# Kernel tuning notes

Hardware: AMD Instinct MI355X
Metric: run time of the kernel (lower is better)

The kernel has to match this reference:

```python
import jax, jax.numpy as jnp
import numpy as np

N_NODES = 50000
N_EDGES = 800000
IN_DIM_N = 128
IN_DIM_E = 32
OUT_DIM = 128


def setup_inputs() -> dict:
    key = jax.random.key(0)
    k = jax.random.split(key, 6)
    nfeats = jax.random.normal(k[0], (N_NODES, IN_DIM_N), dtype=jnp.float32)
    efeats = jax.random.normal(k[1], (N_EDGES, IN_DIM_E), dtype=jnp.float32)
    # xavier-normal-ish scaling
    W_fc = jax.random.normal(k[2], (OUT_DIM, IN_DIM_N), dtype=jnp.float32) * (2.0 / np.sqrt(IN_DIM_N + OUT_DIM))
    W_attn = jax.random.normal(k[3], (1, 2 * OUT_DIM + IN_DIM_E), dtype=jnp.float32) * 0.08
    src = jax.random.randint(k[4], (N_EDGES,), 0, N_NODES, dtype=jnp.int32)
    dst = jax.random.randint(k[5], (N_EDGES,), 0, N_NODES, dtype=jnp.int32)
    return {"nfeats": nfeats, "efeats": efeats, "W_fc": W_fc, "W_attn": W_attn, "src": src, "dst": dst}


def reference(nfeats, efeats, W_fc, W_attn, src, dst):
    n_nodes = nfeats.shape[0]
    out_dim = W_fc.shape[0]
    in_dim_e = efeats.shape[1]

    # z = fc(nfeats)  [N, out_dim]
    z = nfeats @ W_fc.T

    # attn_fc(cat([z_src, efeats, z_dst])) split into three small dots
    a = W_attn[0]
    a_src = a[:out_dim]
    a_e = a[out_dim:out_dim + in_dim_e]
    a_dst = a[out_dim + in_dim_e:]
    s_src = z @ a_src            # [N]
    s_dst = z @ a_dst            # [N]
    s_e = efeats @ a_e           # [E]

    # per-edge attention logit + leaky_relu (torch default slope 0.01)
    e = jax.nn.leaky_relu(s_src[src] + s_e + s_dst[dst], negative_slope=0.01)  # [E]

    # segment softmax over incoming edges of each dst node
    m = jax.ops.segment_max(e, dst, num_segments=n_nodes)
    m = jnp.where(jnp.isfinite(m), m, 0.0)  # guard zero-degree nodes
    w = jnp.exp(e - m[dst])
    denom = jax.ops.segment_sum(w, dst, num_segments=n_nodes)
    alpha = w / jnp.where(denom > 0, denom, 1.0)[dst]  # [E]

    # weighted sum of source z into dst nodes
    h = jax.ops.segment_sum(alpha[:, None] * z[src], dst, num_segments=n_nodes)  # [N, out_dim]
    return h
```

## Files before the change

kernel.cpp:

```cpp
#include <hip/hip_runtime.h>
#include <math.h>

#define N_NODES 50000
#define N_EDGES 800000
#define IN_DIM_N 128
#define IN_DIM_E 32
#define OUT_DIM 128
#define SCAN_BLOCKS ((N_NODES + 255) / 256)
#define GEMM_BLOCKS ((N_NODES + 63) / 64)

typedef __bf16 bf16x8 __attribute__((ext_vector_type(8)));
typedef float  f32x4  __attribute__((ext_vector_type(4)));

__device__ inline unsigned bf16_rne(float x) {
    unsigned u = __float_as_uint(x);
    return (u + 0x7FFFu + ((u >> 16) & 1u)) >> 16;
}
__device__ inline unsigned pack_bf2(float a, float b) {
    return bf16_rne(a) | (bf16_rne(b) << 16);
}

__global__ void wfrag_kernel(const float* __restrict__ W, unsigned* __restrict__ Wfrag,
                             int* __restrict__ counts) {
    int t = blockIdx.x * 256 + threadIdx.x;
    for (int i = t; i < N_NODES; i += 2048) counts[i] = 0;
    if (t >= 2048) return;
    int lane = t & 63;
    int tile = (t >> 6) & 7;
    int ks   = t >> 9;
    int n  = tile * 16 + (lane & 15);
    int kb = ks * 32 + (lane >> 4) * 8;
    const float* srcp = W + n * 128 + kb;
    unsigned o[4];
#pragma unroll
    for (int j = 0; j < 4; ++j) o[j] = pack_bf2(srcp[2 * j], srcp[2 * j + 1]);
    ((uint4*)Wfrag)[t] = *(uint4*)o;
}

__global__ void hist_kernel(const int* __restrict__ dst, int* __restrict__ counts) {
    int i = blockIdx.x * blockDim.x + threadIdx.x;
    if (i < N_EDGES) atomicAdd(&counts[dst[i]], 1);
}

__launch_bounds__(256)
__global__ void gemm_mfma_kernel(const float* __restrict__ A, const unsigned* __restrict__ Wfrag,
                                 const float* __restrict__ attn, unsigned* __restrict__ zb,
                                 float* __restrict__ s_src, float* __restrict__ s_dst) {
    __shared__ unsigned Au[64 * 68];
    __shared__ float asrc[128], adst[128];
    int tid = threadIdx.x;
    int row0 = blockIdx.x * 64;

    if (tid < 128) { asrc[tid] = attn[tid]; adst[tid] = attn[160 + tid]; }

    for (int i = tid; i < 64 * 32; i += 256) {
        int r = i >> 5, q = i & 31;
        int gr = row0 + r;
        float4 v = make_float4(0.f, 0.f, 0.f, 0.f);
        if (gr < N_NODES) v = ((const float4*)A)[(long)gr * 32 + q];
        uint2 p = make_uint2(pack_bf2(v.x, v.y), pack_bf2(v.z, v.w));
        *((uint2*)&Au[r * 68 + q * 2]) = p;
    }
    __syncthreads();

    int lane = tid & 63;
    int wave = tid >> 6;
    int m = lane & 15, quad = lane >> 4;
    const uint4* Wg = (const uint4*)Wfrag;

    f32x4 acc[8];
#pragma unroll
    for (int t = 0; t < 8; ++t) acc[t] = (f32x4){0.f, 0.f, 0.f, 0.f};

#pragma unroll
    for (int ks = 0; ks < 4; ++ks) {
        uint4 au = *((const uint4*)&Au[(wave * 16 + m) * 68 + ks * 16 + quad * 4]);
        bf16x8 af = *(bf16x8*)&au;
#pragma unroll
        for (int t = 0; t < 8; ++t) {
            uint4 bu = Wg[(ks * 8 + t) * 64 + lane];
            bf16x8 bf = *(bf16x8*)&bu;
            acc[t] = __builtin_amdgcn_mfma_f32_16x16x32_bf16(af, bf, acc[t], 0, 0, 0);
        }
    }

    float ps[4] = {0.f, 0.f, 0.f, 0.f}, pd[4] = {0.f, 0.f, 0.f, 0.f};
#pragma unroll
    for (int t = 0; t < 8; ++t) {
        float as_ = asrc[t * 16 + m], ad_ = adst[t * 16 + m];
#pragma unroll
        for (int r = 0; r < 4; ++r) {
            float v = acc[t][r];
            ps[r] = fmaf(v, as_, ps[r]);
            pd[r] = fmaf(v, ad_, pd[r]);
            float vn = __shfl_xor(v, 1, 64);
            if (!(m & 1)) {
                int grow = row0 + wave * 16 + quad * 4 + r;
                if (grow < N_NODES)
                    zb[(long)grow * 64 + t * 8 + (m >> 1)] = pack_bf2(v, vn);
            }
        }
    }
#pragma unroll
    for (int r = 0; r < 4; ++r) {
        for (int off = 1; off < 16; off <<= 1) {
            ps[r] += __shfl_xor(ps[r], off, 64);
            pd[r] += __shfl_xor(pd[r], off, 64);
        }
    }
    if (m == 0) {
#pragma unroll
        for (int r = 0; r < 4; ++r) {
            int grow = row0 + wave * 16 + quad * 4 + r;
            if (grow < N_NODES) { s_src[grow] = ps[r]; s_dst[grow] = pd[r]; }
        }
    }
}

__launch_bounds__(256)
__global__ void scan1_kernel(const int* __restrict__ counts, int* __restrict__ offsets,
                             int* __restrict__ cursor, int* __restrict__ blocksums) {
    int i = blockIdx.x * 256 + threadIdx.x;
    int v = (i < N_NODES) ? counts[i] : 0;
    int lane = threadIdx.x & 63;
    int wv = threadIdx.x >> 6;
    int x = v;
    for (int off = 1; off < 64; off <<= 1) {
        int y = __shfl_up(x, off, 64);
        if (lane >= off) x += y;
    }
    __shared__ int wsum[4];
    if (lane == 63) wsum[wv] = x;
    __syncthreads();
    int base = 0;
    for (int w = 0; w < wv; ++w) base += wsum[w];
    int excl = base + x - v;
    if (i <= N_NODES) offsets[i] = excl;
    if (i < N_NODES) cursor[i] = excl;
    if (threadIdx.x == 255) blocksums[blockIdx.x] = base + x;
}

__launch_bounds__(256)
__global__ void scan2_kernel(int* __restrict__ blocksums) {
    int t = threadIdx.x;
    int v = (t < SCAN_BLOCKS) ? blocksums[t] : 0;
    int lane = t & 63;
    int wv = t >> 6;
    int x = v;
    for (int off = 1; off < 64; off <<= 1) {
        int y = __shfl_up(x, off, 64);
        if (lane >= off) x += y;
    }
    __shared__ int wsum[4];
    if (lane == 63) wsum[wv] = x;
    __syncthreads();
    int base = 0;
    for (int w = 0; w < wv; ++w) base += wsum[w];
    if (t < SCAN_BLOCKS) blocksums[t] = base + x - v;
}

__global__ void score_scatter_kernel(const float* __restrict__ efeats, const float* __restrict__ attn,
                                     const int* __restrict__ src, const int* __restrict__ dst,
                                     const float* __restrict__ s_src, const float* __restrict__ s_dst,
                                     int* __restrict__ cursor, const int* __restrict__ blocksums,
                                     unsigned* __restrict__ pairs4) {
    int i = blockIdx.x * blockDim.x + threadIdx.x;
    if (i >= N_EDGES) return;
    const float4* ef = (const float4*)(efeats + (long)i * IN_DIM_E);
    const float4* ae = (const float4*)(attn + OUT_DIM);
    float se = 0.f;
#pragma unroll
    for (int q = 0; q < IN_DIM_E / 4; ++q) {
        float4 v = ef[q];
        float4 a = ae[q];
        se += v.x * a.x + v.y * a.y + v.z * a.z + v.w * a.w;
    }
    int s = src[i], d = dst[i];
    float x = s_src[s] + se + s_dst[d];
    float ev = (x >= 0.f) ? x : 0.01f * x;
    float w = expf(ev);
    int pos = atomicAdd(&cursor[d], 1) + blocksums[d >> 8];
    pairs4[pos] = (unsigned)s | (bf16_rne(w) << 16);
}

__launch_bounds__(256)
__global__ void aggregate_kernel(const unsigned* __restrict__ pairs4, const int* __restrict__ offsets,
                                 const int* __restrict__ blocksums,
                                 const unsigned* __restrict__ zb, float* __restrict__ h) {
    int node = blockIdx.x * 4 + (threadIdx.x >> 6);
    if (node >= N_NODES) return;
    int lane = threadIdx.x & 63;
    int beg = offsets[node] + blocksums[node >> 8];
    int end = offsets[node + 1] + blocksums[(node + 1) >> 8];
    float ax0 = 0.f, ay0 = 0.f, ax1 = 0.f, ay1 = 0.f;
    float ax2 = 0.f, ay2 = 0.f, ax3 = 0.f, ay3 = 0.f;
    float dsum = 0.f;
    for (int base = beg; base < end; base += 64) {
        int n = min(64, end - base);
        unsigned u = 0;
        if (lane < n) {
            u = pairs4[base + lane];
            dsum += __uint_as_float(u & 0xFFFF0000u);
        }
        int j = 0;
        for (; j + 3 < n; j += 4) {
            unsigned u0 = (unsigned)__shfl((int)u, j, 64);
            unsigned u1 = (unsigned)__shfl((int)u, j + 1, 64);
            unsigned u2 = (unsigned)__shfl((int)u, j + 2, 64);
            unsigned u3 = (unsigned)__shfl((int)u, j + 3, 64);
            unsigned z0 = zb[(long)(u0 & 0xFFFFu) * 64 + lane];
            unsigned z1 = zb[(long)(u1 & 0xFFFFu) * 64 + lane];
            unsigned z2 = zb[(long)(u2 & 0xFFFFu) * 64 + lane];
            unsigned z3 = zb[(long)(u3 & 0xFFFFu) * 64 + lane];
            float w0 = __uint_as_float(u0 & 0xFFFF0000u);
            float w1 = __uint_as_float(u1 & 0xFFFF0000u);
            float w2 = __uint_as_float(u2 & 0xFFFF0000u);
            float w3 = __uint_as_float(u3 & 0xFFFF0000u);
            ax0 = fmaf(w0, __uint_as_float(z0 << 16), ax0);
            ay0 = fmaf(w0, __uint_as_float(z0 & 0xFFFF0000u), ay0);
            ax1 = fmaf(w1, __uint_as_float(z1 << 16), ax1);
            ay1 = fmaf(w1, __uint_as_float(z1 & 0xFFFF0000u), ay1);
            ax2 = fmaf(w2, __uint_as_float(z2 << 16), ax2);
            ay2 = fmaf(w2, __uint_as_float(z2 & 0xFFFF0000u), ay2);
            ax3 = fmaf(w3, __uint_as_float(z3 << 16), ax3);
            ay3 = fmaf(w3, __uint_as_float(z3 & 0xFFFF0000u), ay3);
        }
        for (; j < n; ++j) {
            unsigned u0 = (unsigned)__shfl((int)u, j, 64);
            unsigned z0 = zb[(long)(u0 & 0xFFFFu) * 64 + lane];
            float w0 = __uint_as_float(u0 & 0xFFFF0000u);
            ax0 = fmaf(w0, __uint_as_float(z0 << 16), ax0);
            ay0 = fmaf(w0, __uint_as_float(z0 & 0xFFFF0000u), ay0);
        }
    }
    float accx = (ax0 + ax1) + (ax2 + ax3);
    float accy = (ay0 + ay1) + (ay2 + ay3);
    for (int off = 32; off; off >>= 1) dsum += __shfl_xor(dsum, off, 64);
    float scale = 1.f / (dsum > 0.f ? dsum : 1.f);
    ((float2*)h)[(long)node * 64 + lane] = make_float2(accx * scale, accy * scale);
}

extern "C" void kernel_launch(void* const* d_in, const int* in_sizes, int n_in,
                              void* d_out, int out_size, void* d_ws, size_t ws_size,
                              hipStream_t stream) {
    const float* nfeats = (const float*)d_in[0];
    const float* efeats = (const float*)d_in[1];
    const float* W_fc   = (const float*)d_in[2];
    const float* W_attn = (const float*)d_in[3];
    const int*   src    = (const int*)d_in[4];
    const int*   dst    = (const int*)d_in[5];
    float* h = (float*)d_out;

    char* ws = (char*)d_ws;
    unsigned* zb     = (unsigned*)ws;
    float* s_src     = (float*)(ws + (size_t)N_NODES * 64 * 4);
    float* s_dst     = s_src + N_NODES;
    unsigned* Wfrag  = (unsigned*)(s_dst + N_NODES);
    int*   counts    = (int*)(Wfrag + 8192);
    int*   offsets   = counts + N_NODES;
    int*   cursor    = offsets + N_NODES + 4;
    int*   blocksums = cursor + N_NODES;
    unsigned* pairs4 = (unsigned*)(blocksums + SCAN_BLOCKS + 4);

    wfrag_kernel<<<8, 256, 0, stream>>>(W_fc, Wfrag, counts);
    hist_kernel<<<(N_EDGES + 255) / 256, 256, 0, stream>>>(dst, counts);
    gemm_mfma_kernel<<<GEMM_BLOCKS, 256, 0, stream>>>(
        nfeats, Wfrag, W_attn, zb, s_src, s_dst);
    scan1_kernel<<<SCAN_BLOCKS, 256, 0, stream>>>(counts, offsets, cursor, blocksums);
    scan2_kernel<<<1, 256, 0, stream>>>(blocksums);
    score_scatter_kernel<<<(N_EDGES + 255) / 256, 256, 0, stream>>>(
        efeats, W_attn, src, dst, s_src, s_dst, cursor, blocksums, pairs4);
    aggregate_kernel<<<(N_NODES + 3) / 4, 256, 0, stream>>>(pairs4, offsets, blocksums, zb, h);
}
```

Before: 309.1 us.

## Fuse edge scoring with histogram and record ranks for atomic-free scatter

```diff
diff --git a/kernel.cpp b/kernel.cpp
--- a/kernel.cpp
+++ b/kernel.cpp
@@ -37,11 +37,6 @@
     ((uint4*)Wfrag)[t] = *(uint4*)o;
 }
 
-__global__ void hist_kernel(const int* __restrict__ dst, int* __restrict__ counts) {
-    int i = blockIdx.x * blockDim.x + threadIdx.x;
-    if (i < N_EDGES) atomicAdd(&counts[dst[i]], 1);
-}
-
 __launch_bounds__(256)
 __global__ void gemm_mfma_kernel(const float* __restrict__ A, const unsigned* __restrict__ Wfrag,
                                  const float* __restrict__ attn, unsigned* __restrict__ zb,
@@ -117,9 +112,33 @@
     }
 }
 
+__global__ void edge_score_hist_kernel(const float* __restrict__ efeats, const float* __restrict__ attn,
+                                       const int* __restrict__ src, const int* __restrict__ dst,
+                                       const float* __restrict__ s_src, const float* __restrict__ s_dst,
+                                       int* __restrict__ counts, unsigned short* __restrict__ ranks,
+                                       unsigned short* __restrict__ wq) {
+    int i = blockIdx.x * blockDim.x + threadIdx.x;
+    if (i >= N_EDGES) return;
+    const float4* ef = (const float4*)(efeats + (long)i * IN_DIM_E);
+    const float4* ae = (const float4*)(attn + OUT_DIM);
+    float se = 0.f;
+#pragma unroll
+    for (int q = 0; q < IN_DIM_E / 4; ++q) {
+        float4 v = ef[q];
+        float4 a = ae[q];
+        se += v.x * a.x + v.y * a.y + v.z * a.z + v.w * a.w;
+    }
+    int s = src[i], d = dst[i];
+    float x = s_src[s] + se + s_dst[d];
+    float ev = (x >= 0.f) ? x : 0.01f * x;
+    float w = expf(ev);
+    wq[i] = (unsigned short)bf16_rne(w);
+    ranks[i] = (unsigned short)atomicAdd(&counts[d], 1);
+}
+
 __launch_bounds__(256)
 __global__ void scan1_kernel(const int* __restrict__ counts, int* __restrict__ offsets,
-                             int* __restrict__ cursor, int* __restrict__ blocksums) {
+                             int* __restrict__ blocksums) {
     int i = blockIdx.x * 256 + threadIdx.x;
     int v = (i < N_NODES) ? counts[i] : 0;
     int lane = threadIdx.x & 63;
@@ -136,7 +155,6 @@
     for (int w = 0; w < wv; ++w) base += wsum[w];
     int excl = base + x - v;
     if (i <= N_NODES) offsets[i] = excl;
-    if (i < N_NODES) cursor[i] = excl;
     if (threadIdx.x == 255) blocksums[blockIdx.x] = base + x;
 }
 
@@ -159,28 +177,16 @@
     if (t < SCAN_BLOCKS) blocksums[t] = base + x - v;
 }
 
-__global__ void score_scatter_kernel(const float* __restrict__ efeats, const float* __restrict__ attn,
-                                     const int* __restrict__ src, const int* __restrict__ dst,
-                                     const float* __restrict__ s_src, const float* __restrict__ s_dst,
-                                     int* __restrict__ cursor, const int* __restrict__ blocksums,
-                                     unsigned* __restrict__ pairs4) {
+__global__ void scatter_kernel(const int* __restrict__ src, const int* __restrict__ dst,
+                               const unsigned short* __restrict__ ranks,
+                               const unsigned short* __restrict__ wq,
+                               const int* __restrict__ offsets, const int* __restrict__ blocksums,
+                               unsigned* __restrict__ pairs4) {
     int i = blockIdx.x * blockDim.x + threadIdx.x;
     if (i >= N_EDGES) return;
-    const float4* ef = (const float4*)(efeats + (long)i * IN_DIM_E);
-    const float4* ae = (const float4*)(attn + OUT_DIM);
-    float se = 0.f;
-#pragma unroll
-    for (int q = 0; q < IN_DIM_E / 4; ++q) {
-        float4 v = ef[q];
-        float4 a = ae[q];
-        se += v.x * a.x + v.y * a.y + v.z * a.z + v.w * a.w;
-    }
-    int s = src[i], d = dst[i];
-    float x = s_src[s] + se + s_dst[d];
-    float ev = (x >= 0.f) ? x : 0.01f * x;
-    float w = expf(ev);
-    int pos = atomicAdd(&cursor[d], 1) + blocksums[d >> 8];
-    pairs4[pos] = (unsigned)s | (bf16_rne(w) << 16);
+    int d = dst[i];
+    int pos = offsets[d] + blocksums[d >> 8] + (int)ranks[i];
+    pairs4[pos] = (unsigned)src[i] | ((unsigned)wq[i] << 16);
 }
 
 __launch_bounds__(256)
@@ -258,17 +264,19 @@
     unsigned* Wfrag  = (unsigned*)(s_dst + N_NODES);
     int*   counts    = (int*)(Wfrag + 8192);
     int*   offsets   = counts + N_NODES;
-    int*   cursor    = offsets + N_NODES + 4;
-    int*   blocksums = cursor + N_NODES;
-    unsigned* pairs4 = (unsigned*)(blocksums + SCAN_BLOCKS + 4);
+    int*   blocksums = offsets + N_NODES + 4;
+    unsigned short* ranks = (unsigned short*)(blocksums + SCAN_BLOCKS + 4);
+    unsigned short* wq    = ranks + N_EDGES;
+    unsigned* pairs4      = (unsigned*)(wq + N_EDGES);
 
     wfrag_kernel<<<8, 256, 0, stream>>>(W_fc, Wfrag, counts);
-    hist_kernel<<<(N_EDGES + 255) / 256, 256, 0, stream>>>(dst, counts);
     gemm_mfma_kernel<<<GEMM_BLOCKS, 256, 0, stream>>>(
         nfeats, Wfrag, W_attn, zb, s_src, s_dst);
-    scan1_kernel<<<SCAN_BLOCKS, 256, 0, stream>>>(counts, offsets, cursor, blocksums);
+    edge_score_hist_kernel<<<(N_EDGES + 255) / 256, 256, 0, stream>>>(
+        efeats, W_attn, src, dst, s_src, s_dst, counts, ranks, wq);
+    scan1_kernel<<<SCAN_BLOCKS, 256, 0, stream>>>(counts, offsets, blocksums);
     scan2_kernel<<<1, 256, 0, stream>>>(blocksums);
-    score_scatter_kernel<<<(N_EDGES + 255) / 256, 256, 0, stream>>>(
-        efeats, W_attn, src, dst, s_src, s_dst, cursor, blocksums, pairs4);
+    scatter_kernel<<<(N_EDGES + 255) / 256, 256, 0, stream>>>(
+        src, dst, ranks, wq, offsets, blocksums, pairs4);
     aggregate_kernel<<<(N_NODES + 3) / 4, 256, 0, stream>>>(pairs4, offsets, blocksums, zb, h);
 }
```

Result: faster. 259.5 us (-16.0%).
